# Kernel tuning notes

Hardware: AMD Instinct MI355X
Metric: run time of the kernel (lower is better)

Reference implementation:

```python
import jax, jax.numpy as jnp
import numpy as np

N_NODES = 15000
N_EDGES = 60000
D_NODE_IN = 74
D_EDGE_IN = 12
D = 64            # node_out_feats
D_EHID = 128      # edge_hidden_feats
N_STEPS = 6
BN_EPS = 1e-5


def setup_inputs() -> dict:
    key = jax.random.key(0)
    ks = jax.random.split(key, 16)
    def lin(k, fan_in, shape):
        return jax.random.normal(k, shape, jnp.float32) / np.sqrt(fan_in)
    inp = {
        "node_feats": jax.random.normal(ks[0], (N_NODES, D_NODE_IN), jnp.float32),
        "edge_feats": jax.random.normal(ks[1], (N_EDGES, D_EDGE_IN), jnp.float32),
        "src": jax.random.randint(ks[2], (N_EDGES,), 0, N_NODES, jnp.int32),
        "dst": jax.random.randint(ks[3], (N_EDGES,), 0, N_NODES, jnp.int32),
        # project_node_feats: Linear(node_in, D)
        "W_proj": lin(ks[4], D_NODE_IN, (D_NODE_IN, D)),
        "b_proj": jnp.zeros((D,), jnp.float32),
        # edge network: Linear(edge_in, ehid) -> ReLU -> Linear(ehid, D*D)
        "W_e1": lin(ks[5], D_EDGE_IN, (D_EDGE_IN, D_EHID)),
        "b_e1": jnp.zeros((D_EHID,), jnp.float32),
        "W_e2": lin(ks[6], D_EHID, (D_EHID, D * D)),
        "b_e2": jnp.zeros((D * D,), jnp.float32),
        # NNConv bias + BatchNorm affine params
        "conv_bias": jnp.zeros((D,), jnp.float32),
        "bn_gamma": jnp.ones((D,), jnp.float32),
        "bn_beta": jnp.zeros((D,), jnp.float32),
        # GRU (single layer): torch layout W_ih [3D, D], W_hh [3D, D]
        "W_ih": lin(ks[7], D, (3 * D, D)),
        "W_hh": lin(ks[8], D, (3 * D, D)),
        "b_ih": jnp.zeros((3 * D,), jnp.float32),
        "b_hh": jnp.zeros((3 * D,), jnp.float32),
    }
    return inp


def reference(node_feats, edge_feats, W_proj, b_proj, W_e1, b_e1, W_e2, b_e2,
              conv_bias, bn_gamma, bn_beta, W_ih, W_hh, b_ih, b_hh, src, dst):
    n_nodes = node_feats.shape[0]

    # project_node_feats: Linear + ReLU
    h = jax.nn.relu(node_feats @ W_proj + b_proj)          # [N, D]
    hidden = h                                              # GRU hidden state

    # edge MLP is a pure function of static edge_feats -> compute once
    ew = jax.nn.relu(edge_feats @ W_e1 + b_e1) @ W_e2 + b_e2
    ew = ew.reshape(-1, D, D)                               # [E, D, D]

    # mean-aggregation normalizer (DGL mean: 0 for isolated nodes)
    deg = jax.ops.segment_sum(jnp.ones_like(dst, jnp.float32), dst,
                              num_segments=n_nodes)
    inv_deg = jnp.where(deg > 0, 1.0 / jnp.maximum(deg, 1.0), 0.0)[:, None]

    for _ in range(N_STEPS):
        # per-edge matvec message: (h_src^T W_e); sum over d_in commutes
        # with the mean reduction, so reduce vectors instead of matrices.
        msg = jnp.einsum('ei,eio->eo', h[src], ew)          # [E, D]
        rst = jax.ops.segment_sum(msg, dst, num_segments=n_nodes) * inv_deg
        rst = rst + conv_bias
        # BatchNorm1d (training mode: batch statistics, biased variance)
        mu = rst.mean(axis=0)
        var = rst.var(axis=0)
        rst = (rst - mu) * jax.lax.rsqrt(var + BN_EPS) * bn_gamma + bn_beta
        m = jax.nn.relu(rst)
        # GRU cell (torch gate order: r, z, n)
        gi = m @ W_ih.T + b_ih
        gh = hidden @ W_hh.T + b_hh
        i_r, i_z, i_n = jnp.split(gi, 3, axis=-1)
        h_r, h_z, h_n = jnp.split(gh, 3, axis=-1)
        r = jax.nn.sigmoid(i_r + h_r)
        z = jax.nn.sigmoid(i_z + h_z)
        n = jnp.tanh(i_n + r * h_n)
        hidden = (1.0 - z) * n + z * hidden
        h = hidden
    return h
```

## Files before the change

kernel.cpp:

```cpp
#include <hip/hip_runtime.h>
#include <hip/hip_bf16.h>
#include <math.h>

#define NN 15000
#define NE 60000
#define DIN 74
#define DEIN 12
#define DD 64
#define EH 128
#define NG 8192
#define NSTEPS 6
#define NRB 235
#define NGB 235
#define KAB 384
#define NTMAX 18752
#define NFB 586

typedef unsigned short ushort_t;
typedef __attribute__((ext_vector_type(8))) short short8v;
typedef __attribute__((ext_vector_type(4))) float float4v;

__device__ __forceinline__ float bsf(unsigned short u){
  union { unsigned int i; float f; } v; v.i = ((unsigned int)u) << 16; return v.f;
}
__device__ __forceinline__ unsigned short fsb(float f){
  union { float f; unsigned int i; } v; v.f = f;
  unsigned int x = v.i;
  return (unsigned short)((x + 0x7FFFu + ((x >> 16) & 1u)) >> 16);
}
__device__ __forceinline__ unsigned int pkbf(float a, float b){
  __hip_bfloat162 r = __float22bfloat162_rn(make_float2(a, b));
  union { __hip_bfloat162 h; unsigned int u; } v; v.h = r; return v.u;
}

__global__ void k_sniff(const ushort_t* __restrict__ nf16,
                        const int* __restrict__ dsti, int* __restrict__ flags){
  __shared__ int cnt[2];
  int t = threadIdx.x;
  if (t < 2) cnt[t] = 0;
  __syncthreads();
  int bad = 0;
  for (int i = t; i < 1024; i += 256){
    unsigned short u = nf16[2*i];
    int e = (u >> 7) & 0xFF;
    if (e < 96 || e > 159) bad++;
  }
  if (bad) atomicAdd(&cnt[0], bad);
  if (t < 256 && dsti[2*t+1] == 0) atomicAdd(&cnt[1], 1);
  __syncthreads();
  if (t == 0){
    flags[0] = (cnt[0] > 300) ? 1 : 0;
    flags[1] = (cnt[1] > 250) ? 1 : 0;
  }
}

struct CanonArgs {
  const void* in[15];
  float* out[15];
  int n[15];
};
__global__ void k_canon_all(CanonArgs a, const int* __restrict__ flags){
  int j = blockIdx.y;
  int n = a.n[j];
  int fp32 = flags[0];
  const void* in = a.in[j];
  float* out = a.out[j];
  for (int i = blockIdx.x*256 + threadIdx.x; i < n; i += gridDim.x*256){
    if (fp32) out[i] = ((const float*)in)[i];
    else      out[i] = bsf(((const ushort_t*)in)[i]);
  }
}
__global__ void k_canoni(const void* __restrict__ in, int* __restrict__ out,
                         int n, const int* __restrict__ flags){
  int i = blockIdx.x*256 + threadIdx.x;
  if (i >= n) return;
  long long v = flags[1] ? ((const long long*)in)[i]
                         : (long long)((const int*)in)[i];
  int vi = (int)v;
  if (vi < 0) vi = 0;
  if (vi >= NN) vi = NN-1;
  out[i] = vi;
}

__global__ void k_proj(const float* __restrict__ nf, const float* __restrict__ Wp,
                       const float* __restrict__ bp, float* __restrict__ hid,
                       ushort_t* __restrict__ ab){
  __shared__ float nfl[4][DIN];
  int t = threadIdx.x, blk = blockIdx.x;
  for (int idx = t; idx < 4*DIN; idx += 256){
    int vl = idx / DIN, i = idx - vl*DIN;
    nfl[vl][i] = nf[(size_t)(blk*4+vl)*DIN + i];
  }
  __syncthreads();
  int vl = t >> 6, o = t & 63;
  int v = blk*4 + vl;
  float acc = bp[o];
  for (int i = 0; i < DIN; ++i) acc += nfl[vl][i] * Wp[i*DD + o];
  float r = fmaxf(acc, 0.f);
  hid[(size_t)v*DD + o] = r;
  ushort_t hh = fsb(r);
  float hl = r - bsf(hh);
  ab[(size_t)v*KAB + 64 + o]  = hh;
  ab[(size_t)v*KAB + 192 + o] = fsb(hl);
  ab[(size_t)v*KAB + 320 + o] = hh;
}

__global__ void k_emlp(const float* __restrict__ ef, const float* __restrict__ W1,
                       const float* __restrict__ b1, ushort_t* __restrict__ thi,
                       ushort_t* __restrict__ tlo){
  __shared__ float efl[2][DEIN];
  int t = threadIdx.x, blk = blockIdx.x;
  if (t < 2*DEIN){
    int el = t / DEIN, i = t - el*DEIN;
    efl[el][i] = ef[(size_t)(blk*2+el)*DEIN + i];
  }
  __syncthreads();
  int el = t >> 7, c = t & 127;
  float acc = b1[c];
  for (int i = 0; i < DEIN; ++i) acc += efl[el][i] * W1[i*EH + c];
  float tv = fmaxf(acc, 0.f);
  ushort_t hiv = fsb(tv);
  size_t off = (size_t)(blk*2+el)*EH + c;
  thi[off] = hiv;
  tlo[off] = fsb(tv - bsf(hiv));
}
__global__ void k_zpad(ushort_t* __restrict__ thi, ushort_t* __restrict__ tlo){
  int t = threadIdx.x;
  thi[(size_t)NE*EH + t] = 0;
  tlo[(size_t)NE*EH + t] = 0;
}

__global__ void k_w2q(const float* __restrict__ W2, const float* __restrict__ b2,
                      ushort_t* __restrict__ w2q, ushort_t* __restrict__ w2b){
  int idx = blockIdx.x*256 + threadIdx.x;
  if (idx < NG*DD){
    int n = idx >> 6, i = idx & 63;
    int kq = n >> 11, rem = n & 2047;
    int o = rem >> 5, kl = rem & 31;
    int kg = kq*32 + kl;
    w2q[idx] = fsb(W2[(size_t)kg*4096 + i*64 + o]);
  } else if (idx < NG*DD + DD*DD){
    int r = idx - NG*DD;
    int o = r >> 6, i = r & 63;
    w2b[r] = fsb(b2[i*64 + o]);
  }
}

__global__ void k_wgru(const float* __restrict__ Wih, const float* __restrict__ Whh,
                       ushort_t* __restrict__ wg){
  int pos = blockIdx.x*256 + threadIdx.x;
  if (pos >= 256*KAB) return;
  int c = pos / KAB, k = pos - c*KAB;
  int kb = k >> 6, i = k & 63;
  int g = c >> 6, o = c & 63;
  float w = 0.f;
  if ((kb & 1) == 0){
    if (g == 0)      w = Wih[(size_t)(o)*64 + i];
    else if (g == 1) w = Wih[(size_t)(64+o)*64 + i];
    else if (g == 2) w = Wih[(size_t)(128+o)*64 + i];
  } else {
    if (g == 0)      w = Whh[(size_t)(o)*64 + i];
    else if (g == 1) w = Whh[(size_t)(64+o)*64 + i];
    else if (g == 3) w = Whh[(size_t)(128+o)*64 + i];
  }
  ushort_t hi = fsb(w);
  wg[pos] = (kb >= 4) ? fsb(w - bsf(hi)) : hi;
}

__global__ void k_zero(int* __restrict__ p, int n){
  int i = blockIdx.x*256 + threadIdx.x;
  if (i < n) p[i] = 0;
}
__global__ void k_deg(const int* __restrict__ idxarr, int* __restrict__ deg){
  int e = blockIdx.x*256 + threadIdx.x;
  if (e < NE) atomicAdd(&deg[idxarr[e]], 1);
}
__global__ void k_scan(const int* __restrict__ deg, int* __restrict__ rowp,
                       float* __restrict__ invd){
  __shared__ int ssum[256];
  int t = threadIdx.x;
  const int STRIP = (NN + 255) / 256;
  int lo = t*STRIP, hi = (lo + STRIP < NN) ? lo + STRIP : NN;
  int s = 0;
  for (int i = lo; i < hi; ++i) s += deg[i];
  ssum[t] = s;
  __syncthreads();
  if (t == 0){
    int acc = 0;
    for (int i = 0; i < 256; ++i){ int v = ssum[i]; ssum[i] = acc; acc += v; }
  }
  __syncthreads();
  int acc = ssum[t];
  for (int i = lo; i < hi; ++i){
    rowp[i] = acc;
    int d = deg[i];
    invd[i] = (d > 0) ? 1.0f/(float)d : 0.0f;
    acc += d;
  }
  if (t == 255) rowp[NN] = acc;
}
__global__ void k_scatter(const int* __restrict__ idxarr, const int* __restrict__ rowp,
                          int* __restrict__ cursor, int* __restrict__ eidx,
                          int* __restrict__ epos){
  int e = blockIdx.x*256 + threadIdx.x;
  if (e < NE){
    int d = idxarr[e];
    int pos = atomicAdd(&cursor[d], 1);
    int slot = rowp[d] + pos;
    eidx[slot] = e;
    if (epos) epos[e] = slot;
  }
}

__global__ void k_tiles(const int* __restrict__ rowp, int* __restrict__ tnode,
                        int* __restrict__ tbase, int* __restrict__ tcnt,
                        int* __restrict__ ntb){
  __shared__ int ss[256];
  int t = threadIdx.x;
  const int STRIP = (NN + 255) / 256;
  int lo = t*STRIP, hi = lo + STRIP; if (hi > NN) hi = NN;
  int c = 0;
  for (int i = lo; i < hi; ++i){
    int deg = rowp[i+1] - rowp[i];
    c += (deg + 15) >> 4;
  }
  ss[t] = c;
  __syncthreads();
  if (t == 0){
    int a = 0;
    for (int i = 0; i < 256; ++i){ int v = ss[i]; ss[i] = a; a += v; }
    ntb[0] = a;
  }
  __syncthreads();
  int pos = ss[t];
  for (int i = lo; i < hi; ++i){
    int b = rowp[i], deg = rowp[i+1] - b;
    for (int r = 0; r < deg; r += 16){
      tnode[pos] = i; tbase[pos] = b + r;
      int c2 = deg - r; tcnt[pos] = (c2 > 16) ? 16 : c2;
      ++pos;
    }
  }
}

__global__ __launch_bounds__(512,4) void k_fused7(
    const ushort_t* __restrict__ ab, const ushort_t* __restrict__ w2q,
    const ushort_t* __restrict__ w2b, const ushort_t* __restrict__ thi,
    const ushort_t* __restrict__ tlo,
    const int* __restrict__ tnode, const int* __restrict__ tbase,
    const int* __restrict__ tcnt, const int* __restrict__ ntb,
    const int* __restrict__ eidx, const int* __restrict__ epos,
    float* __restrict__ msg){
  __shared__ __align__(16) ushort_t Gl[32768];
  __shared__ float bhl[32*66];
  __shared__ int nodl[32], cntl[32], basel[32];
  __shared__ int eidl[32][16];
  __shared__ int posl[32][16];

  int tid = threadIdx.x;
  int nt = ntb[0];
  int T0 = blockIdx.x * 32;
  if (T0 >= nt) return;
  int wv = tid >> 6, lane = tid & 63;
  int lr = lane & 15, quad = lane >> 4;

  if (tid < 32){
    int gt = T0 + tid;
    int node = 0, base = 0, cnt = 0;
    if (gt < nt){ node = tnode[gt]; base = tbase[gt]; cnt = tcnt[gt]; }
    nodl[tid] = node; basel[tid] = base; cntl[tid] = cnt;
  }
  __syncthreads();
  {
    int j = tid >> 4, sl = tid & 15;
    int eid = NE, ps = 0;
    if (sl < cntl[j]){
      eid = eidx[basel[j] + sl];
      ps = epos[eid];
    }
    eidl[j][sl] = eid;
    posl[j][sl] = ps;
  }
  short8v hf0k0, hf0k1, hf1k0, hf1k1;
  {
    int n0 = nodl[lr], n1 = nodl[16 + lr];
    hf0k0 = *(const short8v*)(ab + (size_t)n0*KAB + 64 + quad*8);
    hf0k1 = *(const short8v*)(ab + (size_t)n0*KAB + 96 + quad*8);
    hf1k0 = *(const short8v*)(ab + (size_t)n1*KAB + 64 + quad*8);
    hf1k1 = *(const short8v*)(ab + (size_t)n1*KAB + 96 + quad*8);
  }
  {
    int ot = wv & 3, mh = wv >> 2;
    float4v ba = (float4v){0.f,0.f,0.f,0.f};
    short8v a0 = *(const short8v*)(w2b + (size_t)(ot*16 + lr)*DD + quad*8);
    short8v a1 = *(const short8v*)(w2b + (size_t)(ot*16 + lr)*DD + 32 + quad*8);
    ba = __builtin_amdgcn_mfma_f32_16x16x32_bf16(a0, mh ? hf1k0 : hf0k0, ba, 0,0,0);
    ba = __builtin_amdgcn_mfma_f32_16x16x32_bf16(a1, mh ? hf1k1 : hf0k1, ba, 0,0,0);
    #pragma unroll
    for (int reg = 0; reg < 4; ++reg)
      bhl[(mh*16 + lr)*66 + ot*16 + quad*4 + reg] = ba[reg];
  }

  int j0 = wv*4;
  for (int oh = 0; oh < 2; ++oh){
    float4v acc[4][2];
    #pragma unroll
    for (int j = 0; j < 4; ++j)
      #pragma unroll
      for (int ot = 0; ot < 2; ++ot)
        acc[j][ot] = (float4v){0.f,0.f,0.f,0.f};
    for (int kq = 0; kq < 4; ++kq){
      __syncthreads();
      #pragma unroll 4
      for (int it = 0; it < 8; ++it){
        int tile = wv*8 + it;
        int nrow = kq*2048 + oh*1024 + tile*16 + lr;
        const ushort_t* arow = w2q + (size_t)nrow*DD;
        short8v a0 = *(const short8v*)(arow + quad*8);
        short8v a1 = *(const short8v*)(arow + 32 + quad*8);
        int ol = tile >> 1;
        int klb = ((tile & 1) << 4) + quad*4;
        int q8 = klb >> 3, jj = klb & 7;
        #pragma unroll
        for (int mh = 0; mh < 2; ++mh){
          float4v g = (float4v){0.f,0.f,0.f,0.f};
          g = __builtin_amdgcn_mfma_f32_16x16x32_bf16(a0, mh ? hf1k0 : hf0k0, g, 0,0,0);
          g = __builtin_amdgcn_mfma_f32_16x16x32_bf16(a1, mh ? hf1k1 : hf0k1, g, 0,0,0);
          int m = mh*16 + lr;
          unsigned int p0 = pkbf(g[0], g[1]);
          unsigned int p1 = pkbf(g[2], g[3]);
          int byt = ((((m*4 + q8)*32 + ol) << 4) + jj*2) ^ ((m & 7) << 4);
          uint2 pv; pv.x = p0; pv.y = p1;
          *(uint2*)((char*)Gl + byt) = pv;
        }
      }
      short8v th0, th1, th2, th3, tw0, tw1, tw2, tw3;
      {
        size_t kqo = (size_t)kq*32 + quad*8;
        int e0 = eidl[j0+0][lr], e1 = eidl[j0+1][lr];
        int e2 = eidl[j0+2][lr], e3 = eidl[j0+3][lr];
        th0 = *(const short8v*)(thi + (size_t)e0*EH + kqo);
        tw0 = *(const short8v*)(tlo + (size_t)e0*EH + kqo);
        th1 = *(const short8v*)(thi + (size_t)e1*EH + kqo);
        tw1 = *(const short8v*)(tlo + (size_t)e1*EH + kqo);
        th2 = *(const short8v*)(thi + (size_t)e2*EH + kqo);
        tw2 = *(const short8v*)(tlo + (size_t)e2*EH + kqo);
        th3 = *(const short8v*)(thi + (size_t)e3*EH + kqo);
        tw3 = *(const short8v*)(tlo + (size_t)e3*EH + kqo);
      }
      __syncthreads();
      #pragma unroll
      for (int j = 0; j < 4; ++j){
        int m = j0 + j;
        int swz = (m & 7) << 4;
        short8v thj = (j==0)?th0:(j==1)?th1:(j==2)?th2:th3;
        short8v twj = (j==0)?tw0:(j==1)?tw1:(j==2)?tw2:tw3;
        #pragma unroll
        for (int ot = 0; ot < 2; ++ot){
          int byt = (((m*4 + quad)*32 + ot*16 + lr) << 4) ^ swz;
          short8v gf = *(const short8v*)((const char*)Gl + byt);
          acc[j][ot] = __builtin_amdgcn_mfma_f32_16x16x32_bf16(thj, gf, acc[j][ot], 0,0,0);
          acc[j][ot] = __builtin_amdgcn_mfma_f32_16x16x32_bf16(twj, gf, acc[j][ot], 0,0,0);
        }
      }
    }
    #pragma unroll
    for (int j = 0; j < 4; ++j){
      int m = j0 + j;
      #pragma unroll
      for (int ot = 0; ot < 2; ++ot){
        int o = oh*32 + ot*16 + lr;
        float bb = bhl[m*66 + o];
        #pragma unroll
        for (int reg = 0; reg < 4; ++reg){
          int sl = quad*4 + reg;
          int eid = eidl[m][sl];
          if (eid < NE) msg[(size_t)posl[m][sl]*DD + o] = acc[j][ot][reg] + bb;
        }
      }
    }
  }
}

__global__ void k_red(const float* __restrict__ msg, const int* __restrict__ rowp_d,
                      const float* __restrict__ invd, const float* __restrict__ cbias,
                      float* __restrict__ rst, float* __restrict__ part){
  __shared__ float ls[256], ls2[256];
  int t = threadIdx.x, blk = blockIdx.x;
  int o = t & 63, gg = t >> 6;
  float cb = cbias[o];
  float s = 0.f, s2 = 0.f;
  #pragma unroll 1
  for (int j = 0; j < 16; ++j){
    int n = blk*64 + gg*16 + j;
    if (n >= NN) break;
    int b = rowp_d[n], e = rowp_d[n+1];
    float a0 = 0.f, a1 = 0.f, a2 = 0.f, a3 = 0.f;
    int i = b;
    for (; i + 3 < e; i += 4){
      a0 += msg[(size_t)i*DD + o];
      a1 += msg[(size_t)(i+1)*DD + o];
      a2 += msg[(size_t)(i+2)*DD + o];
      a3 += msg[(size_t)(i+3)*DD + o];
    }
    for (; i < e; ++i) a0 += msg[(size_t)i*DD + o];
    float x = ((a0 + a1) + (a2 + a3)) * invd[n] + cb;
    rst[(size_t)n*DD + o] = x;
    s += x; s2 += x*x;
  }
  ls[t] = s; ls2[t] = s2;
  __syncthreads();
  if (gg == 0){
    part[blk*128 + o]      = ls[o] + ls[64+o] + ls[128+o] + ls[192+o];
    part[blk*128 + 64 + o] = ls2[o] + ls2[64+o] + ls2[128+o] + ls2[192+o];
  }
}

__global__ void k_bnf(const float* __restrict__ part, const float* __restrict__ gamma,
                      const float* __restrict__ beta, float* __restrict__ stats){
  __shared__ float sh[128];
  int t = threadIdx.x;
  float s0 = 0.f, s1 = 0.f, s2 = 0.f, s3 = 0.f;
  int b = 0;
  for (; b + 3 < NRB; b += 4){
    s0 += part[b*128 + t];
    s1 += part[(b+1)*128 + t];
    s2 += part[(b+2)*128 + t];
    s3 += part[(b+3)*128 + t];
  }
  for (; b < NRB; ++b) s0 += part[b*128 + t];
  sh[t] = (s0 + s1) + (s2 + s3);
  __syncthreads();
  if (t < 64){
    float mu = sh[t] / (float)NN;
    float var = sh[64+t] / (float)NN - mu*mu;
    if (var < 0.f) var = 0.f;
    float rsq = rsqrtf(var + 1e-5f);
    float scl = rsq * gamma[t];
    stats[t] = scl;
    stats[64 + t] = beta[t] - mu*scl;
  }
}

__global__ __launch_bounds__(512) void k_gru_one(
    const float* __restrict__ rst, const float* __restrict__ stats,
    ushort_t* __restrict__ ab, const ushort_t* __restrict__ wg,
    const float* __restrict__ bih, const float* __restrict__ bhh,
    float* __restrict__ hid, float* __restrict__ out, int write_out){
  __shared__ __align__(16) ushort_t As[64][136];
  __shared__ __align__(16) ushort_t Bs[256][136];
  __shared__ float gl[64*257];
  __shared__ float scl[64], sft[64];
  int t = threadIdx.x;
  int r0 = blockIdx.x * 64;
  if (t < 64){ scl[t] = stats[t]; sft[t] = stats[64+t]; }
  int wv = t >> 6, lane = t & 63;
  int lr = lane & 15, quad = lane >> 4;
  int n0 = wv * 32;
  float4v acc[4][2];
  #pragma unroll
  for (int mt = 0; mt < 4; ++mt)
    #pragma unroll
    for (int nt = 0; nt < 2; ++nt) acc[mt][nt] = (float4v){0.f,0.f,0.f,0.f};
  for (int kt = 0; kt < 3; ++kt){
    __syncthreads();
    #pragma unroll
    for (int it = 0; it < 2; ++it){
      int cid = t + it*512;
      int r = cid >> 4, ko = (cid & 15) * 8;
      int gm = r0 + r; if (gm >= NN) gm = NN-1;
      if (ko < 64){
        float4 x0 = *(const float4*)(rst + (size_t)gm*DD + ko);
        float4 x1 = *(const float4*)(rst + (size_t)gm*DD + ko + 4);
        float xv[8] = {x0.x,x0.y,x0.z,x0.w,x1.x,x1.y,x1.z,x1.w};
        ushort_t u[8];
        #pragma unroll
        for (int jj = 0; jj < 8; ++jj){
          float m = fmaxf(xv[jj]*scl[ko+jj] + sft[ko+jj], 0.f);
          ushort_t mh = fsb(m);
          u[jj] = (kt == 1) ? fsb(m - bsf(mh)) : mh;
        }
        *(uint4*)&As[r][ko] = *(const uint4*)u;
      } else {
        *(uint4*)&As[r][ko] = *(const uint4*)(ab + (size_t)gm*KAB + kt*128 + ko);
      }
    }
    #pragma unroll
    for (int it = 0; it < 8; ++it){
      int cid = t + it*512;
      int rB = cid >> 4, ko = (cid & 15) * 8;
      *(uint4*)&Bs[rB][ko] = *(const uint4*)(wg + (size_t)rB*KAB + kt*128 + ko);
    }
    __syncthreads();
    #pragma unroll
    for (int ks = 0; ks < 4; ++ks){
      short8v a[4];
      #pragma unroll
      for (int mt = 0; mt < 4; ++mt)
        a[mt] = *(const short8v*)&As[mt*16 + lr][ks*32 + quad*8];
      #pragma unroll
      for (int nt = 0; nt < 2; ++nt){
        short8v b = *(const short8v*)&Bs[n0 + nt*16 + lr][ks*32 + quad*8];
        #pragma unroll
        for (int mt = 0; mt < 4; ++mt)
          acc[mt][nt] = __builtin_amdgcn_mfma_f32_16x16x32_bf16(a[mt], b, acc[mt][nt], 0,0,0);
      }
    }
  }
  #pragma unroll
  for (int mt = 0; mt < 4; ++mt)
    #pragma unroll
    for (int nt = 0; nt < 2; ++nt){
      int col = n0 + nt*16 + lr;
      #pragma unroll
      for (int reg = 0; reg < 4; ++reg)
        gl[(mt*16 + quad*4 + reg)*257 + col] = acc[mt][nt][reg];
    }
  __syncthreads();
  for (int idx = t; idx < 64*64; idx += 512){
    int row = idx >> 6, o = idx & 63;
    int v = r0 + row;
    if (v >= NN) break;
    const float* g = &gl[row*257];
    float aR  = g[o]       + bih[o]      + bhh[o];
    float aZ  = g[64 + o]  + bih[64+o]   + bhh[64+o];
    float aNi = g[128 + o] + bih[128+o];
    float aNh = g[192 + o] + bhh[128+o];
    float hprev = hid[(size_t)v*DD + o];
    float r = 1.f/(1.f+__expf(-aR));
    float z = 1.f/(1.f+__expf(-aZ));
    float n = tanhf(aNi + r*aNh);
    float hnew = (1.f - z)*n + z*hprev;
    hid[(size_t)v*DD + o] = hnew;
    ushort_t hh = fsb(hnew);
    float hl = hnew - bsf(hh);
    ab[(size_t)v*KAB + 64 + o]  = hh;
    ab[(size_t)v*KAB + 192 + o] = fsb(hl);
    ab[(size_t)v*KAB + 320 + o] = hh;
    if (write_out) out[(size_t)v*DD + o] = hnew;
  }
}

extern "C" void kernel_launch(void* const* d_in, const int* in_sizes, int n_in,
                              void* d_out, int out_size, void* d_ws, size_t ws_size,
                              hipStream_t stream){
  (void)out_size; (void)ws_size;
  float* out = (float*)d_out;

  int p_nf=-1,p_ef=-1,p_src=-1,p_dst=-1,p_Wp=-1,p_bp=-1,p_W1=-1,p_b1=-1,
      p_W2=-1,p_b2=-1,p_cb=-1,p_gam=-1,p_bet=-1,p_Wih=-1,p_Whh=-1,p_bih=-1,p_bhh=-1;
  int c60000=0,c64=0,c12288=0,c192=0;
  for (int i = 0; i < n_in; ++i){
    switch (in_sizes[i]){
      case 1110000: p_nf = i; break;
      case 720000:  p_ef = i; break;
      case 60000:   if (c60000++ == 0) p_src = i; else p_dst = i; break;
      case 4736:    p_Wp = i; break;
      case 64:      { if (c64==0) p_bp=i; else if (c64==1) p_cb=i;
                      else if (c64==2) p_gam=i; else p_bet=i; c64++; } break;
      case 1536:    p_W1 = i; break;
      case 128:     p_b1 = i; break;
      case 524288:  p_W2 = i; break;
      case 4096:    p_b2 = i; break;
      case 12288:   if (c12288++ == 0) p_Wih = i; else p_Whh = i; break;
      case 192:    if (c192++ == 0) p_bih = i; else p_bhh = i; break;
      default: break;
    }
  }

  char* p = (char*)d_ws;
  auto alloc = [&](size_t bytes)->char*{
    char* r = p; p += (bytes + 255) & ~(size_t)255; return r;
  };
  int* flags = (int*)alloc(256);
  const int FPOS[15] = {p_nf,p_ef,p_Wp,p_bp,p_W1,p_b1,p_W2,p_b2,p_cb,p_gam,p_bet,
                        p_Wih,p_Whh,p_bih,p_bhh};
  CanonArgs ca;
  int maxn = 0;
  for (int j = 0; j < 15; ++j){
    int n = in_sizes[FPOS[j]];
    ca.in[j]  = d_in[FPOS[j]];
    ca.out[j] = (float*)alloc((size_t)n * 4);
    ca.n[j]   = n;
    if (n > maxn) maxn = n;
  }
  const float* nf  = ca.out[0];  const float* ef  = ca.out[1];
  const float* Wp  = ca.out[2];  const float* bp  = ca.out[3];
  const float* W1  = ca.out[4];  const float* b1  = ca.out[5];
  const float* W2  = ca.out[6];  const float* b2  = ca.out[7];
  const float* cb  = ca.out[8];  const float* gam = ca.out[9];
  const float* bet = ca.out[10]; const float* Wih = ca.out[11];
  const float* Whh = ca.out[12]; const float* bih = ca.out[13];
  const float* bhh = ca.out[14];
  int* srcc = (int*)alloc((size_t)NE*4);
  int* dstc = (int*)alloc((size_t)NE*4);

  ushort_t* thi   = (ushort_t*)alloc((size_t)(NE+1)*EH*2);
  ushort_t* tlo   = (ushort_t*)alloc((size_t)(NE+1)*EH*2);
  ushort_t* w2q   = (ushort_t*)alloc((size_t)NG*DD*2);
  ushort_t* w2b   = (ushort_t*)alloc((size_t)DD*DD*2);
  float* hid      = (float*)alloc((size_t)NN*DD*4);
  ushort_t* ab    = (ushort_t*)alloc((size_t)NN*KAB*2);
  ushort_t* wg    = (ushort_t*)alloc((size_t)256*KAB*2);
  float* rst      = (float*)alloc((size_t)NN*DD*4);
  float* msg      = (float*)alloc((size_t)NE*DD*4);
  float* part     = (float*)alloc((size_t)NRB*128*4);
  float* stats    = (float*)alloc(128*4);
  int* degall     = (int*)alloc((size_t)4*NN*4);
  int* deg  = degall;
  int* curd = degall + NN;
  int* deg2 = degall + 2*NN; int* cursor2 = degall + 3*NN;
  float* invd = (float*)alloc((size_t)NN*4);
  int* rowp_d = (int*)alloc((size_t)(NN+1)*4);
  int* eidx_d = (int*)alloc((size_t)NE*4);
  int* epos   = (int*)alloc((size_t)NE*4);
  int* rowp2  = (int*)alloc((size_t)(NN+1)*4);
  float* invd2= (float*)alloc((size_t)NN*4);
  int* eidx2  = (int*)alloc((size_t)NE*4);
  int* tnode  = (int*)alloc((size_t)NTMAX*4);
  int* tbase  = (int*)alloc((size_t)NTMAX*4);
  int* tcnt   = (int*)alloc((size_t)NTMAX*4);
  int* ntb    = (int*)alloc(256);

  k_sniff<<<1, 256, 0, stream>>>((const ushort_t*)d_in[p_nf], (const int*)d_in[p_dst], flags);
  k_canon_all<<<dim3((maxn+255)/256, 15), 256, 0, stream>>>(ca, flags);
  k_canoni<<<(NE+255)/256, 256, 0, stream>>>(d_in[p_src], srcc, NE, flags);
  k_canoni<<<(NE+255)/256, 256, 0, stream>>>(d_in[p_dst], dstc, NE, flags);

  k_proj <<<NN/4,  256, 0, stream>>>(nf, Wp, bp, hid, ab);
  k_emlp <<<NE/2,  256, 0, stream>>>(ef, W1, b1, thi, tlo);
  k_zpad <<<1, 128, 0, stream>>>(thi, tlo);
  k_w2q  <<<(NG*DD + DD*DD + 255)/256, 256, 0, stream>>>(W2, b2, w2q, w2b);
  k_wgru <<<(256*KAB+255)/256, 256, 0, stream>>>(Wih, Whh, wg);
  k_zero <<<(4*NN+255)/256, 256, 0, stream>>>(degall, 4*NN);
  k_deg  <<<(NE+255)/256, 256, 0, stream>>>(dstc, deg);
  k_deg  <<<(NE+255)/256, 256, 0, stream>>>(srcc, deg2);
  k_scan <<<1, 256, 0, stream>>>(deg,  rowp_d, invd);
  k_scan <<<1, 256, 0, stream>>>(deg2, rowp2, invd2);
  k_scatter<<<(NE+255)/256, 256, 0, stream>>>(dstc, rowp_d, curd, eidx_d, epos);
  k_scatter<<<(NE+255)/256, 256, 0, stream>>>(srcc, rowp2, cursor2, eidx2, (int*)0);
  k_tiles<<<1, 256, 0, stream>>>(rowp2, tnode, tbase, tcnt, ntb);

  for (int s = 0; s < NSTEPS; ++s){
    k_fused7<<<NFB, 512, 0, stream>>>(ab, w2q, w2b, thi, tlo,
                                      tnode, tbase, tcnt, ntb, eidx2, epos, msg);
    k_red <<<NRB, 256, 0, stream>>>(msg, rowp_d, invd, cb, rst, part);
    k_bnf <<<1, 128, 0, stream>>>(part, gam, bet, stats);
    k_gru_one<<<NGB, 512, 0, stream>>>(rst, stats, ab, wg, bih, bhh, hid, out,
                                       (s == NSTEPS-1) ? 1 : 0);
  }
}
```

Before: 1.038 ms.

## Fold BatchNorm finalize into GRU kernel and merge paired setup launches

Removes the single-block BN-finalize kernel by having every GRU block redundantly reduce the per-block partial sums into scale and shift. Merges paired src/dst canonicalize, degree, scan and scatter kernels into single launches using a grid y-dimension. Widens the reduction kernel to 512 threads with 8 nodes per thread group. This cuts kernel launches and serialization points per step, at the cost of each of the 235 GRU blocks re-reading all partials.

```diff
diff --git a/kernel.cpp b/kernel.cpp
--- a/kernel.cpp
+++ b/kernel.cpp
@@ -70,10 +70,13 @@
     else      out[i] = bsf(((const ushort_t*)in)[i]);
   }
 }
-__global__ void k_canoni(const void* __restrict__ in, int* __restrict__ out,
-                         int n, const int* __restrict__ flags){
+__global__ void k_canoni2(const void* __restrict__ in0, const void* __restrict__ in1,
+                          int* __restrict__ out0, int* __restrict__ out1,
+                          const int* __restrict__ flags){
   int i = blockIdx.x*256 + threadIdx.x;
-  if (i >= n) return;
+  if (i >= NE) return;
+  const void* in = blockIdx.y ? in1 : in0;
+  int* out = blockIdx.y ? out1 : out0;
   long long v = flags[1] ? ((const long long*)in)[i]
                          : (long long)((const int*)in)[i];
   int vi = (int)v;
@@ -171,12 +174,21 @@
   int i = blockIdx.x*256 + threadIdx.x;
   if (i < n) p[i] = 0;
 }
-__global__ void k_deg(const int* __restrict__ idxarr, int* __restrict__ deg){
+__global__ void k_deg2(const int* __restrict__ a0, const int* __restrict__ a1,
+                       int* __restrict__ d0, int* __restrict__ d1){
   int e = blockIdx.x*256 + threadIdx.x;
-  if (e < NE) atomicAdd(&deg[idxarr[e]], 1);
-}
-__global__ void k_scan(const int* __restrict__ deg, int* __restrict__ rowp,
-                       float* __restrict__ invd){
+  if (e < NE){
+    if (blockIdx.y == 0) atomicAdd(&d0[a0[e]], 1);
+    else                 atomicAdd(&d1[a1[e]], 1);
+  }
+}
+__global__ void k_scan2(const int* __restrict__ degA, int* __restrict__ rowpA,
+                        float* __restrict__ invdA,
+                        const int* __restrict__ degB, int* __restrict__ rowpB,
+                        float* __restrict__ invdB){
+  const int* deg = blockIdx.x ? degB : degA;
+  int* rowp      = blockIdx.x ? rowpB : rowpA;
+  float* invd    = blockIdx.x ? invdB : invdA;
   __shared__ int ssum[256];
   int t = threadIdx.x;
   const int STRIP = (NN + 255) / 256;
@@ -199,16 +211,23 @@
   }
   if (t == 255) rowp[NN] = acc;
 }
-__global__ void k_scatter(const int* __restrict__ idxarr, const int* __restrict__ rowp,
-                          int* __restrict__ cursor, int* __restrict__ eidx,
-                          int* __restrict__ epos){
+__global__ void k_scatter2(const int* __restrict__ dstc, const int* __restrict__ rowpD,
+                           int* __restrict__ curD, int* __restrict__ eidxD,
+                           int* __restrict__ epos,
+                           const int* __restrict__ srcc, const int* __restrict__ rowpS,
+                           int* __restrict__ curS, int* __restrict__ eidxS){
   int e = blockIdx.x*256 + threadIdx.x;
-  if (e < NE){
-    int d = idxarr[e];
-    int pos = atomicAdd(&cursor[d], 1);
-    int slot = rowp[d] + pos;
-    eidx[slot] = e;
-    if (epos) epos[e] = slot;
+  if (e >= NE) return;
+  if (blockIdx.y == 0){
+    int d = dstc[e];
+    int pos = atomicAdd(&curD[d], 1);
+    int slot = rowpD[d] + pos;
+    eidxD[slot] = e;
+    epos[e] = slot;
+  } else {
+    int d = srcc[e];
+    int pos = atomicAdd(&curS[d], 1);
+    eidxS[rowpS[d] + pos] = e;
   }
 }
 
@@ -382,17 +401,18 @@
   }
 }
 
-__global__ void k_red(const float* __restrict__ msg, const int* __restrict__ rowp_d,
+__global__ __launch_bounds__(512) void k_red(const float* __restrict__ msg,
+                      const int* __restrict__ rowp_d,
                       const float* __restrict__ invd, const float* __restrict__ cbias,
                       float* __restrict__ rst, float* __restrict__ part){
-  __shared__ float ls[256], ls2[256];
+  __shared__ float ls[512], ls2[512];
   int t = threadIdx.x, blk = blockIdx.x;
   int o = t & 63, gg = t >> 6;
   float cb = cbias[o];
   float s = 0.f, s2 = 0.f;
   #pragma unroll 1
-  for (int j = 0; j < 16; ++j){
-    int n = blk*64 + gg*16 + j;
+  for (int j = 0; j < 8; ++j){
+    int n = blk*64 + gg*8 + j;
     if (n >= NN) break;
     int b = rowp_d[n], e = rowp_d[n+1];
     float a0 = 0.f, a1 = 0.f, a2 = 0.f, a3 = 0.f;
@@ -410,40 +430,23 @@
   }
   ls[t] = s; ls2[t] = s2;
   __syncthreads();
-  if (gg == 0){
-    part[blk*128 + o]      = ls[o] + ls[64+o] + ls[128+o] + ls[192+o];
-    part[blk*128 + 64 + o] = ls2[o] + ls2[64+o] + ls2[128+o] + ls2[192+o];
-  }
-}
-
-__global__ void k_bnf(const float* __restrict__ part, const float* __restrict__ gamma,
-                      const float* __restrict__ beta, float* __restrict__ stats){
-  __shared__ float sh[128];
-  int t = threadIdx.x;
-  float s0 = 0.f, s1 = 0.f, s2 = 0.f, s3 = 0.f;
-  int b = 0;
-  for (; b + 3 < NRB; b += 4){
-    s0 += part[b*128 + t];
-    s1 += part[(b+1)*128 + t];
-    s2 += part[(b+2)*128 + t];
-    s3 += part[(b+3)*128 + t];
-  }
-  for (; b < NRB; ++b) s0 += part[b*128 + t];
-  sh[t] = (s0 + s1) + (s2 + s3);
-  __syncthreads();
   if (t < 64){
-    float mu = sh[t] / (float)NN;
-    float var = sh[64+t] / (float)NN - mu*mu;
-    if (var < 0.f) var = 0.f;
-    float rsq = rsqrtf(var + 1e-5f);
-    float scl = rsq * gamma[t];
-    stats[t] = scl;
-    stats[64 + t] = beta[t] - mu*scl;
+    float a = 0.f;
+    #pragma unroll
+    for (int g = 0; g < 8; ++g) a += ls[g*64 + t];
+    part[blk*128 + t] = a;
+  } else if (t < 128){
+    int o2 = t - 64;
+    float a = 0.f;
+    #pragma unroll
+    for (int g = 0; g < 8; ++g) a += ls2[g*64 + o2];
+    part[blk*128 + 64 + o2] = a;
   }
 }
 
 __global__ __launch_bounds__(512) void k_gru_one(
-    const float* __restrict__ rst, const float* __restrict__ stats,
+    const float* __restrict__ rst, const float* __restrict__ part,
+    const float* __restrict__ gamma, const float* __restrict__ beta,
     ushort_t* __restrict__ ab, const ushort_t* __restrict__ wg,
     const float* __restrict__ bih, const float* __restrict__ bhh,
     float* __restrict__ hid, float* __restrict__ out, int write_out){
@@ -451,9 +454,31 @@
   __shared__ __align__(16) ushort_t Bs[256][136];
   __shared__ float gl[64*257];
   __shared__ float scl[64], sft[64];
+  __shared__ float sh[128];
   int t = threadIdx.x;
   int r0 = blockIdx.x * 64;
-  if (t < 64){ scl[t] = stats[t]; sft[t] = stats[64+t]; }
+  if (t < 128){
+    float s0 = 0.f, s1 = 0.f, s2 = 0.f, s3 = 0.f;
+    int b = 0;
+    for (; b + 3 < NRB; b += 4){
+      s0 += part[b*128 + t];
+      s1 += part[(b+1)*128 + t];
+      s2 += part[(b+2)*128 + t];
+      s3 += part[(b+3)*128 + t];
+    }
+    for (; b < NRB; ++b) s0 += part[b*128 + t];
+    sh[t] = (s0 + s1) + (s2 + s3);
+  }
+  __syncthreads();
+  if (t < 64){
+    float mu = sh[t] / (float)NN;
+    float var = sh[64+t] / (float)NN - mu*mu;
+    if (var < 0.f) var = 0.f;
+    float rsq = rsqrtf(var + 1e-5f);
+    float sc = rsq * gamma[t];
+    scl[t] = sc;
+    sft[t] = beta[t] - mu*sc;
+  }
   int wv = t >> 6, lane = t & 63;
   int lr = lane & 15, quad = lane >> 4;
   int n0 = wv * 32;
@@ -605,7 +630,6 @@
   float* rst      = (float*)alloc((size_t)NN*DD*4);
   float* msg      = (float*)alloc((size_t)NE*DD*4);
   float* part     = (float*)alloc((size_t)NRB*128*4);
-  float* stats    = (float*)alloc(128*4);
   int* degall     = (int*)alloc((size_t)4*NN*4);
   int* deg  = degall;
   int* curd = degall + NN;
@@ -624,8 +648,8 @@
 
   k_sniff<<<1, 256, 0, stream>>>((const ushort_t*)d_in[p_nf], (const int*)d_in[p_dst], flags);
   k_canon_all<<<dim3((maxn+255)/256, 15), 256, 0, stream>>>(ca, flags);
-  k_canoni<<<(NE+255)/256, 256, 0, stream>>>(d_in[p_src], srcc, NE, flags);
-  k_canoni<<<(NE+255)/256, 256, 0, stream>>>(d_in[p_dst], dstc, NE, flags);
+  k_canoni2<<<dim3((NE+255)/256, 2), 256, 0, stream>>>(d_in[p_src], d_in[p_dst],
+                                                       srcc, dstc, flags);
 
   k_proj <<<NN/4,  256, 0, stream>>>(nf, Wp, bp, hid, ab);
   k_emlp <<<NE/2,  256, 0, stream>>>(ef, W1, b1, thi, tlo);
@@ -633,20 +657,17 @@
   k_w2q  <<<(NG*DD + DD*DD + 255)/256, 256, 0, stream>>>(W2, b2, w2q, w2b);
   k_wgru <<<(256*KAB+255)/256, 256, 0, stream>>>(Wih, Whh, wg);
   k_zero <<<(4*NN+255)/256, 256, 0, stream>>>(degall, 4*NN);
-  k_deg  <<<(NE+255)/256, 256, 0, stream>>>(dstc, deg);
-  k_deg  <<<(NE+255)/256, 256, 0, stream>>>(srcc, deg2);
-  k_scan <<<1, 256, 0, stream>>>(deg,  rowp_d, invd);
-  k_scan <<<1, 256, 0, stream>>>(deg2, rowp2, invd2);
-  k_scatter<<<(NE+255)/256, 256, 0, stream>>>(dstc, rowp_d, curd, eidx_d, epos);
-  k_scatter<<<(NE+255)/256, 256, 0, stream>>>(srcc, rowp2, cursor2, eidx2, (int*)0);
+  k_deg2 <<<dim3((NE+255)/256, 2), 256, 0, stream>>>(dstc, srcc, deg, deg2);
+  k_scan2<<<2, 256, 0, stream>>>(deg, rowp_d, invd, deg2, rowp2, invd2);
+  k_scatter2<<<dim3((NE+255)/256, 2), 256, 0, stream>>>(dstc, rowp_d, curd, eidx_d,
+                                                        epos, srcc, rowp2, cursor2, eidx2);
   k_tiles<<<1, 256, 0, stream>>>(rowp2, tnode, tbase, tcnt, ntb);
 
   for (int s = 0; s < NSTEPS; ++s){
     k_fused7<<<NFB, 512, 0, stream>>>(ab, w2q, w2b, thi, tlo,
                                       tnode, tbase, tcnt, ntb, eidx2, epos, msg);
-    k_red <<<NRB, 256, 0, stream>>>(msg, rowp_d, invd, cb, rst, part);
-    k_bnf <<<1, 128, 0, stream>>>(part, gam, bet, stats);
-    k_gru_one<<<NGB, 512, 0, stream>>>(rst, stats, ab, wg, bih, bhh, hid, out,
-                                       (s == NSTEPS-1) ? 1 : 0);
-  }
-}
+    k_red <<<NRB, 512, 0, stream>>>(msg, rowp_d, invd, cb, rst, part);
+    k_gru_one<<<NGB, 512, 0, stream>>>(rst, part, gam, bet, ab, wg, bih, bhh,
+                                       hid, out, (s == NSTEPS-1) ? 1 : 0);
+  }
+}
```

Measured after the change: 944.2 us, median of 3. 1.1x faster.
